# Optimization experiments

Measured on AMD Instinct MI355X. Metric: run time of the kernel, lower is better.

The kernel has to match this reference:

```python
import jax, jax.numpy as jnp
import numpy as np

HImg = 640
WImg = 640
P = 7            # ROI pool grid (7x7x3 = 147 features)
K = 100          # max detections kept after NMS
CONF_THR = 0.4
IOU_THR = 0.5


def xywh_to_xyxy(b):
    cx, cy, w, h = b[..., 0], b[..., 1], b[..., 2], b[..., 3]
    return jnp.stack([cx - w / 2, cy - h / 2, cx + w / 2, cy + h / 2], axis=-1)


def pairwise_iou(a, b):
    # a: [N,4], b: [M,4] in xyxy
    lt = jnp.maximum(a[:, None, :2], b[None, :, :2])
    rb = jnp.minimum(a[:, None, 2:], b[None, :, 2:])
    wh = jnp.clip(rb - lt, 0.0)
    inter = wh[..., 0] * wh[..., 1]
    area_a = (a[:, 2] - a[:, 0]) * (a[:, 3] - a[:, 1])
    area_b = (b[:, 2] - b[:, 0]) * (b[:, 3] - b[:, 1])
    return inter / (area_a[:, None] + area_b[None, :] - inter + 1e-7)


def nms_single(boxes, scores):
    # class-agnostic greedy NMS, fixed-shape (mask-based)
    N = boxes.shape[0]
    order = jnp.argsort(-scores)
    b = boxes[order]
    s = scores[order]
    iou = pairwise_iou(b, b)           # [N,N]
    valid = s > CONF_THR
    idx = jnp.arange(N)

    def step(supp, i):
        keep_i = valid[i] & ~supp[i]
        supp = supp | (keep_i & (iou[i] > IOU_THR) & (idx > i))
        return supp, None

    supp, _ = jax.lax.scan(step, jnp.zeros(N, dtype=bool), idx)
    keep = valid & ~supp
    return b, s, keep


def roi_pool(img, box):
    # img: [3,H,W], box: [4] xyxy pixels -> [147] nearest-neighbor 7x7 crop
    x1, y1, x2, y2 = box[0], box[1], box[2], box[3]
    xs = x1 + (x2 - x1) * (jnp.arange(P) + 0.5) / P
    ys = y1 + (y2 - y1) * (jnp.arange(P) + 0.5) / P
    xi = jnp.clip(xs, 0, WImg - 1).astype(jnp.int32)
    yi = jnp.clip(ys, 0, HImg - 1).astype(jnp.int32)
    crop = img[:, yi[:, None], xi[None, :]]   # [3,P,P]
    return crop.reshape(-1)


def setup_inputs() -> dict:
    key = jax.random.key(0)
    ks = jax.random.split(key, 10)
    B, N = 16, 1024
    x = jax.random.uniform(ks[0], (B, 3, HImg, WImg), dtype=jnp.float32)
    cxy = jax.random.uniform(ks[1], (B, N, 2), minval=0.0, maxval=640.0)
    wh = jax.random.uniform(ks[2], (B, N, 2), minval=10.0, maxval=200.0)
    conf = jax.random.uniform(ks[3], (B, N, 1))
    cls = jax.random.randint(ks[4], (B, N, 1), 0, 4).astype(jnp.float32)
    dets = jnp.concatenate([cxy, wh, conf, cls], axis=-1)  # [B,N,6] xywh,conf,cls
    W1 = jax.random.normal(ks[5], (147, 255), dtype=jnp.float32) * 0.05
    b1 = jnp.zeros((255,), jnp.float32)
    W2 = jax.random.normal(ks[6], (255, 128), dtype=jnp.float32) * 0.05
    b2 = jnp.zeros((128,), jnp.float32)
    W3 = jax.random.normal(ks[7], (128, 4), dtype=jnp.float32) * 0.05
    b3 = jnp.zeros((4,), jnp.float32)
    return {"x": x, "dets": dets, "W1": W1, "b1": b1, "W2": W2, "b2": b2,
            "W3": W3, "b3": b3}


def reference(x, dets, W1, b1, W2, b2, W3, b3):
    boxes = xywh_to_xyxy(dets[..., :4])      # [B,N,4]
    scores = dets[..., 4]                    # [B,N]
    b, s, keep = jax.vmap(nms_single)(boxes, scores)
    masked = jnp.where(keep, s, -1.0)
    topv, topi = jax.lax.top_k(masked, K)    # [B,K]
    sel_boxes = jnp.take_along_axis(b, topi[..., None], axis=1)  # [B,K,4]
    valid = topv > 0.0                       # kept boxes have conf > 0.4
    # per-detection crop + classify (mobilenet proxy)
    crops = jax.vmap(lambda img, bxs: jax.vmap(lambda bb: roi_pool(img, bb))(bxs))(x, sel_boxes)  # [B,K,147]
    feat = crops @ W1 + b1                   # [B,K,255] mobilenet output proxy
    h = jax.nn.relu(feat @ W2 + b2)          # combine: Linear(255,128)+ReLU
    out = h @ W3 + b3                        # Linear(128,4)
    return jnp.where(valid[..., None], out, 0.0)  # [B,K,4]
```

## Files before the change

### kernel.cpp

```cpp
#include <hip/hip_runtime.h>

#define NBOX 1024
#define KTOP 100
#define CONF_THR 0.4f
#define IOU_THR 0.5f
#define RPB 4
#define G 4
#define CHUNK 480

typedef unsigned long long u64;

__global__ __launch_bounds__(1024) void sort_kernel(
    const float* __restrict__ dets,
    float4* __restrict__ sboxes,
    int* __restrict__ nv_out)
{
    const int b = blockIdx.x, t = threadIdx.x;
    __shared__ float skey[NBOX];
    __shared__ int   sidx[NBOX];
    const float* db = dets + (size_t)b * NBOX * 6;

    const float st = db[t*6+4];
    skey[t] = st;
    sidx[t] = t;
    __syncthreads();

    for (int k = 2; k <= NBOX; k <<= 1) {
        for (int j = k >> 1; j > 0; j >>= 1) {
            int i = t, ixj = i ^ j;
            if (ixj > i) {
                float si = skey[i], sj = skey[ixj];
                int   ai = sidx[i], aj = sidx[ixj];
                bool before = (si > sj) || (si == sj && ai < aj);
                bool want   = ((i & k) == 0);
                if (before != want) {
                    skey[i] = sj; skey[ixj] = si;
                    sidx[i] = aj; sidx[ixj] = ai;
                }
            }
            __syncthreads();
        }
    }

    {
        int oi = sidx[t];
        float cx = db[oi*6+0], cy = db[oi*6+1];
        float w  = db[oi*6+2], h  = db[oi*6+3];
        float hw = __fmul_rn(w, 0.5f), hh = __fmul_rn(h, 0.5f);
        sboxes[(size_t)b*NBOX + t] = make_float4(__fsub_rn(cx,hw), __fsub_rn(cy,hh),
                                                 __fadd_rn(cx,hw), __fadd_rn(cy,hh));
    }
    int cnt = __syncthreads_count(st > CONF_THR);
    if (t == 0) nv_out[b] = cnt;
}

__global__ __launch_bounds__(256) void iou_mask_kernel(
    const float4* __restrict__ sboxes,
    const int* __restrict__ nv,
    u64* __restrict__ mask)
{
    const int b  = blockIdx.y;
    const int i0 = blockIdx.x * RPB;
    const int nvB = nv[b];
    if (i0 >= nvB) return;
    const int tid = threadIdx.x;
    const int lane = tid & 63, wv = tid >> 6;

    const float4* sb = sboxes + (size_t)b * NBOX;
    float4 bi[RPB]; float ai[RPB];
    #pragma unroll
    for (int r = 0; r < RPB; ++r) {
        bi[r] = sb[min(i0 + r, NBOX - 1)];
        ai[r] = __fmul_rn(__fsub_rn(bi[r].z, bi[r].x), __fsub_rn(bi[r].w, bi[r].y));
    }
    u64* rowbase = mask + ((size_t)b * NBOX + i0) * 16;

    for (int c = 0; c < 4; ++c) {
        const int j = c * 256 + tid;
        const float4 bj = sb[j];
        const float aj = __fmul_rn(__fsub_rn(bj.z, bj.x), __fsub_rn(bj.w, bj.y));
        #pragma unroll
        for (int r = 0; r < RPB; ++r) {
            const int i = i0 + r;
            if (i >= nvB) break;
            float lx = fmaxf(bi[r].x, bj.x), ly = fmaxf(bi[r].y, bj.y);
            float rx = fminf(bi[r].z, bj.z), ry = fminf(bi[r].w, bj.w);
            float iw = fmaxf(__fsub_rn(rx, lx), 0.0f);
            float ih = fmaxf(__fsub_rn(ry, ly), 0.0f);
            float inter = __fmul_rn(iw, ih);
            float denom = __fadd_rn(__fsub_rn(__fadd_rn(ai[r], aj), inter), 1e-7f);
            bool pred = (j > i) && (__fdiv_rn(inter, denom) > IOU_THR);
            u64 m = __ballot(pred);
            if (lane == 0) rowbase[(size_t)r * 16 + c * 4 + wv] = m;
        }
    }
}

__global__ __launch_bounds__(1024) void scan_kernel(
    const float4* __restrict__ sboxes,
    const u64* __restrict__ mask,
    const int* __restrict__ nv,
    float4* __restrict__ sel,
    int* __restrict__ nkeep)
{
    const int b = blockIdx.x, tid = threadIdx.x;
    const int lane = tid & 63;
    const int nvB = nv[b];
    const u64* mb = mask + (size_t)b * NBOX * 16;

    __shared__ u64 lm[CHUNK * 16];
    __shared__ int s_stop;

    u64 sw = 0, kw = 0;
    int kcnt = 0;
    if (tid == 0) s_stop = 0;

    for (int base = 0; base < nvB; base += CHUNK) {
        const int cn = min(CHUNK, nvB - base);
        for (int idx = tid; idx < cn * 16; idx += 1024)
            lm[idx] = mb[(size_t)base * 16 + idx];
        __syncthreads();

        if (tid < 64) {
            u64 pre[8];
            #pragma unroll
            for (int u = 0; u < 8; ++u)
                pre[u] = (u < cn && lane < 16) ? lm[u * 16 + lane] : 0ull;
            for (int r0 = 0; r0 < cn && kcnt < KTOP; r0 += 8) {
                #pragma unroll
                for (int u = 0; u < 8; ++u) {
                    const int r = r0 + u;
                    u64 row = pre[u];
                    const int rp = r + 8;
                    pre[u] = (rp < cn && lane < 16) ? lm[rp * 16 + lane] : 0ull;
                    if (r < cn && kcnt < KTOP) {
                        const int i = base + r;
                        const int wsel = i >> 6;
                        u64 sword = __shfl(sw, wsel);
                        if (!((sword >> (i & 63)) & 1ull)) {
                            sw |= row;
                            if (lane == wsel) kw |= (1ull << (i & 63));
                            ++kcnt;
                        }
                    }
                }
            }
            if (tid == 0 && kcnt >= KTOP) s_stop = 1;
        }
        __syncthreads();
        if (s_stop) break;
    }

    if (tid < 64) {
        int cnt = (lane < 16) ? __popcll(kw) : 0;
        int pfx = cnt;
        #pragma unroll
        for (int d = 1; d < 16; d <<= 1) { int t2 = __shfl_up(pfx, d); if (lane >= d) pfx += t2; }
        const int excl = pfx - cnt;
        const int total = __shfl(pfx, 15);

        const float4* sb = sboxes + (size_t)b * NBOX;
        float4* selb = sel + (size_t)b * KTOP;
        for (int w = 0; w < 16; ++w) {
            u64 kwW = __shfl(kw, w);
            int bR  = __shfl(excl, w);
            if ((kwW >> lane) & 1ull) {
                int rank = bR + __popcll(kwW & ((1ull << lane) - 1ull));
                if (rank < KTOP) selb[rank] = sb[w * 64 + lane];
            }
        }
        for (int r = total + lane; r < KTOP; r += 64) selb[r] = make_float4(0,0,0,0);
        if (lane == 0) nkeep[b] = total < KTOP ? total : KTOP;
    }
}

__global__ __launch_bounds__(256) void roi_mlp_kernel(
    const float* __restrict__ x,
    const float4* __restrict__ sel,
    const int* __restrict__ nkeep,
    const float* __restrict__ W1, const float* __restrict__ b1,
    const float* __restrict__ W2, const float* __restrict__ b2,
    const float* __restrict__ W3, const float* __restrict__ b3,
    float* __restrict__ out)
{
    const int b = blockIdx.y, k0 = blockIdx.x * G, tid = threadIdx.x;
    __shared__ float crop[G][147];
    __shared__ float feat[G][255];
    __shared__ float hb[G][128];
    const int nvB = nkeep[b];
    const float4* selb = sel + (size_t)b * KTOP;

    for (int task = tid; task < G * 147; task += 256) {
        int g = task / 147, r = task - g * 147;
        int c = r / 49, rr = r - c * 49;
        int py = rr / 7, px = rr - py * 7;
        float4 bb = selb[k0 + g];
        float fx = __fadd_rn(bb.x, __fdiv_rn(__fmul_rn(__fsub_rn(bb.z, bb.x), (float)px + 0.5f), 7.0f));
        float fy = __fadd_rn(bb.y, __fdiv_rn(__fmul_rn(__fsub_rn(bb.w, bb.y), (float)py + 0.5f), 7.0f));
        int xi = (int)fminf(fmaxf(fx, 0.0f), 639.0f);
        int yi = (int)fminf(fmaxf(fy, 0.0f), 639.0f);
        crop[g][r] = x[(((size_t)b * 3 + c) * 640 + yi) * 640 + xi];
    }
    __syncthreads();

    if (tid < 255) {
        float a0 = b1[tid], a1 = a0, a2 = a0, a3 = a0;
        for (int i = 0; i < 147; ++i) {
            float w = W1[i * 255 + tid];
            a0 += crop[0][i] * w; a1 += crop[1][i] * w;
            a2 += crop[2][i] * w; a3 += crop[3][i] * w;
        }
        feat[0][tid] = a0; feat[1][tid] = a1; feat[2][tid] = a2; feat[3][tid] = a3;
    }
    __syncthreads();

    {
        const int col = tid & 127, g0 = (tid >> 7) * 2;
        float a0 = b2[col], a1 = a0;
        for (int i = 0; i < 255; ++i) {
            float w = W2[i * 128 + col];
            a0 += feat[g0][i] * w; a1 += feat[g0 + 1][i] * w;
        }
        hb[g0][col] = fmaxf(a0, 0.0f); hb[g0 + 1][col] = fmaxf(a1, 0.0f);
    }
    __syncthreads();

    if (tid < 4 * G) {
        const int g = tid >> 2, o = tid & 3;
        float acc = b3[o];
        for (int i = 0; i < 128; ++i) acc += hb[g][i] * W3[i * 4 + o];
        const int k = k0 + g;
        out[((size_t)b * KTOP + k) * 4 + o] = (k < nvB) ? acc : 0.0f;
    }
}

extern "C" void kernel_launch(void* const* d_in, const int* in_sizes, int n_in,
                              void* d_out, int out_size, void* d_ws, size_t ws_size,
                              hipStream_t stream) {
    const float* x    = (const float*)d_in[0];
    const float* dets = (const float*)d_in[1];
    const float* W1   = (const float*)d_in[2];
    const float* b1   = (const float*)d_in[3];
    const float* W2   = (const float*)d_in[4];
    const float* b2   = (const float*)d_in[5];
    const float* W3   = (const float*)d_in[6];
    const float* b3   = (const float*)d_in[7];
    float* out = (float*)d_out;

    const int B = in_sizes[1] / (NBOX * 6);

    float4* sboxes = (float4*)d_ws;
    float4* sel    = sboxes + (size_t)B * NBOX;
    u64*    mask   = (u64*)(sel + (size_t)B * KTOP);
    int*    nv     = (int*)(mask + (size_t)B * NBOX * 16);
    int*    nkeep  = nv + B;

    sort_kernel<<<B, NBOX, 0, stream>>>(dets, sboxes, nv);

    dim3 gmask(NBOX / RPB, B);
    iou_mask_kernel<<<gmask, 256, 0, stream>>>(sboxes, nv, mask);

    scan_kernel<<<B, 1024, 0, stream>>>(sboxes, mask, nv, sel, nkeep);

    dim3 groi(KTOP / G, B);
    roi_mlp_kernel<<<groi, 256, 0, stream>>>(x, sel, nkeep,
                                             W1, b1, W2, b2, W3, b3, out);
}
```

Measured before the change: 189.5 us.

## Use wavefront shuffles for intra-warp bitonic sort stages; retune RPB and CHUNK

The bitonic sort keeps each key/index pair in registers. Stages with stride below 64 use __shfl_xor inside a 64-lane wavefront, and only the larger strides go through shared memory with block barriers. This removes most __syncthreads calls and shared-memory traffic from the sort. The change also doubles rows per block in the IoU mask kernel and shrinks CHUNK, which shifts parallelism and work per block in later kernels.

```diff
diff --git a/kernel.cpp b/kernel.cpp
--- a/kernel.cpp
+++ b/kernel.cpp
@@ -4,9 +4,9 @@
 #define KTOP 100
 #define CONF_THR 0.4f
 #define IOU_THR 0.5f
-#define RPB 4
+#define RPB 8
 #define G 4
-#define CHUNK 480
+#define CHUNK 256
 
 typedef unsigned long long u64;
 
@@ -21,31 +21,44 @@
     const float* db = dets + (size_t)b * NBOX * 6;
 
     const float st = db[t*6+4];
-    skey[t] = st;
-    sidx[t] = t;
-    __syncthreads();
-
-    for (int k = 2; k <= NBOX; k <<= 1) {
+    float mk = st;
+    int   mi = t;
+
+    #pragma unroll
+    for (int k = 2; k <= 64; k <<= 1) {
+        const bool want = ((t & k) == 0);
         for (int j = k >> 1; j > 0; j >>= 1) {
-            int i = t, ixj = i ^ j;
-            if (ixj > i) {
-                float si = skey[i], sj = skey[ixj];
-                int   ai = sidx[i], aj = sidx[ixj];
-                bool before = (si > sj) || (si == sj && ai < aj);
-                bool want   = ((i & k) == 0);
-                if (before != want) {
-                    skey[i] = sj; skey[ixj] = si;
-                    sidx[i] = aj; sidx[ixj] = ai;
-                }
-            }
+            float pk = __shfl_xor(mk, j);
+            int   pi = __shfl_xor(mi, j);
+            bool cmp_mp = (mk > pk) || (mk == pk && mi < pi);
+            bool low = ((t & j) == 0);
+            if ((cmp_mp == want) != low) { mk = pk; mi = pi; }
+        }
+    }
+    for (int k = 128; k <= NBOX; k <<= 1) {
+        const bool want = ((t & k) == 0);
+        for (int j = k >> 1; j >= 64; j >>= 1) {
+            skey[t] = mk; sidx[t] = mi;
             __syncthreads();
+            float pk = skey[t ^ j];
+            int   pi = sidx[t ^ j];
+            bool cmp_mp = (mk > pk) || (mk == pk && mi < pi);
+            bool low = ((t & j) == 0);
+            if ((cmp_mp == want) != low) { mk = pk; mi = pi; }
+            __syncthreads();
+        }
+        for (int j = 32; j > 0; j >>= 1) {
+            float pk = __shfl_xor(mk, j);
+            int   pi = __shfl_xor(mi, j);
+            bool cmp_mp = (mk > pk) || (mk == pk && mi < pi);
+            bool low = ((t & j) == 0);
+            if ((cmp_mp == want) != low) { mk = pk; mi = pi; }
         }
     }
 
     {
-        int oi = sidx[t];
-        float cx = db[oi*6+0], cy = db[oi*6+1];
-        float w  = db[oi*6+2], h  = db[oi*6+3];
+        float cx = db[mi*6+0], cy = db[mi*6+1];
+        float w  = db[mi*6+2], h  = db[mi*6+3];
         float hw = __fmul_rn(w, 0.5f), hh = __fmul_rn(h, 0.5f);
         sboxes[(size_t)b*NBOX + t] = make_float4(__fsub_rn(cx,hw), __fsub_rn(cy,hh),
                                                  __fadd_rn(cx,hw), __fadd_rn(cy,hh));
```

Measured after the change: 184.7 us. 2.6% less time.
